# Kernel tuning notes

Measured on AMD Instinct MI355X. Metric: run time of the kernel, lower is better.

The kernel has to match this reference:

```python
import jax, jax.numpy as jnp
import numpy as np

E, MAX_M, K, N = 8, 2048, 2048, 8192

def setup_inputs() -> dict:
    key = jax.random.key(0)
    k1, k2, k3 = jax.random.split(key, 3)
    x_padded = jax.random.normal(k1, (E, MAX_M, K), dtype=jnp.float32)
    stacked_weights = jax.random.normal(k2, (E, N, K), dtype=jnp.float32) * 0.02
    m_sizes = jax.random.randint(k3, (E,), 0, MAX_M, dtype=jnp.int32)
    return {"x_padded": x_padded, "stacked_weights": stacked_weights, "m_sizes": m_sizes}

def reference(x_padded, stacked_weights, m_sizes):
    # valid-token mask per expert: [E, MAX_M]
    mask = (jnp.arange(MAX_M, dtype=jnp.int32)[None, :] < m_sizes[:, None])
    # zero padded rows (pad_expert_inputs fills with zeros)
    x = jnp.where(mask[:, :, None], x_padded, jnp.zeros((), x_padded.dtype))
    # grouped GEMM via batched matmul: [E, M, K] x [E, N, K]^T -> [E, M, N]
    out = jnp.einsum('emk,enk->emn', x, stacked_weights)
    # rows beyond m_sizes[i] are sliced away in the original; mask them to zero
    return jnp.where(mask[:, :, None], out, jnp.zeros((), out.dtype))
```

## Files before the change

kernel.cpp:

```cpp
#include <hip/hip_runtime.h>
#include <hip/hip_bf16.h>


#define NE   8
#define MAXM 2048
#define KD   2048
#define ND   8192

#define BM   256
#define BN   256
#define BK   64
#define NTS  (KD/BK)

typedef __attribute__((ext_vector_type(8))) short          short8;
typedef __attribute__((ext_vector_type(8))) unsigned short us8;
typedef __attribute__((ext_vector_type(4))) float          f32x4;
typedef __attribute__((ext_vector_type(4))) unsigned short us4;

__device__ __forceinline__ unsigned short f2bf(float f) {
    union { float f; unsigned u; } v; v.f = f;
    unsigned u = v.u;
    return (unsigned short)((u + 0x7FFFu + ((u >> 16) & 1u)) >> 16);
}

__device__ __forceinline__ void gload16(const void* g, void* l) {
    __builtin_amdgcn_global_load_lds(
        (const __attribute__((address_space(1))) void*)g,
        (__attribute__((address_space(3))) void*)l, 16, 0, 0);
}

__global__ __launch_bounds__(256) void cvt_kernel(const float* __restrict__ src,
                                                  unsigned short* __restrict__ dst,
                                                  int n8) {
    int i = blockIdx.x * blockDim.x + threadIdx.x;
    int stride = gridDim.x * blockDim.x;
    for (; i < n8; i += stride) {
        const f32x4* s = (const f32x4*)(src + (size_t)i * 8);
        f32x4 a = s[0], b = s[1];
        us8 v = (us8){f2bf(a[0]), f2bf(a[1]), f2bf(a[2]), f2bf(a[3]),
                      f2bf(b[0]), f2bf(b[1]), f2bf(b[2]), f2bf(b[3])};
        *(us8*)(dst + (size_t)i * 8) = v;
    }
}

__global__ __launch_bounds__(256) void cvt_x_kernel(const float* __restrict__ src,
                                                    unsigned short* __restrict__ dst,
                                                    const int* __restrict__ ms) {
    int bid = blockIdx.x;
    int e = bid >> 11, m = bid & 2047;
    if (m >= ms[e]) return;
    const float* s = src + ((size_t)e * MAXM + m) * KD;
    unsigned short* d = dst + ((size_t)e * MAXM + m) * KD;
    int t = threadIdx.x;
    const f32x4* s4 = (const f32x4*)(s + t * 8);
    f32x4 a = s4[0], b = s4[1];
    us8 v = (us8){f2bf(a[0]), f2bf(a[1]), f2bf(a[2]), f2bf(a[3]),
                  f2bf(b[0]), f2bf(b[1]), f2bf(b[2]), f2bf(b[3])};
    *(us8*)(d + t * 8) = v;
}

__global__ __launch_bounds__(512, 2) void ggemm_pers(
    const unsigned short* __restrict__ xb,
    const unsigned short* __restrict__ wb,
    const int*   __restrict__ ms,
    float*       __restrict__ out)
{
    int p    = blockIdx.x;
    int xcd  = p & 7;
    int q    = p >> 3;
    int rrot = q >> 2;
    int bc   = xcd * 4 + (q & 3);
    int col0 = bc * BN;
    int tid  = threadIdx.x;

    __shared__ int s_live[8];
    __shared__ int s_nlive;
    __shared__ unsigned short Ak[2][2][BM * 32];
    __shared__ unsigned short Bk[2][2][BN * 32];

    if (tid == 0) {
        int n = 0;
        #pragma unroll
        for (int e = 0; e < NE; ++e) {
            int br = (rrot + e) & 7;
            if (br * BM < ms[e]) { s_live[n] = (e << 3) | br; ++n; }
        }
        s_nlive = n;
    }

    #pragma unroll 1
    for (int e = 0; e < NE; ++e) {
        int br   = (rrot + e) & 7;
        int row0 = br * BM;
        if (row0 >= ms[e]) {
            float* outE = out + (size_t)e * MAXM * ND;
            f32x4 z = (f32x4){0.f, 0.f, 0.f, 0.f};
            #pragma unroll
            for (int j = 0; j < 32; ++j) {
                int i2 = tid + j * 512;
                int rr = i2 >> 6, cc = (i2 & 63) << 2;
                *(f32x4*)(outE + (size_t)(row0 + rr) * ND + col0 + cc) = z;
            }
        }
    }
    __syncthreads();
    int nlive = s_nlive;
    if (nlive == 0) return;

    int wid = tid >> 6, lane = tid & 63;
    int wr = wid >> 2, wc = wid & 3;
    int lr = lane & 15, kg = lane >> 4;
    int srow = lane >> 2;
    int ss   = (lane & 3) ^ ((lane >> 3) & 3);

    auto stageA = [&](int b, int kh, const unsigned short* xP, int kt) {
        #pragma unroll
        for (int j = 0; j < 2; ++j) {
            int blk = wid * 2 + j;
            const unsigned short* src =
                xP + (size_t)(blk * 16 + srow) * KD + kt * BK + kh * 32 + ss * 8;
            gload16(src, (char*)&Ak[b][kh][0] + blk * 1024);
        }
    };
    auto stageB = [&](int b, int kh, const unsigned short* wP, int kt) {
        #pragma unroll
        for (int j = 0; j < 2; ++j) {
            int blk = wid * 2 + j;
            const unsigned short* src =
                wP + (size_t)(blk * 16 + srow) * KD + kt * BK + kh * 32 + ss * 8;
            gload16(src, (char*)&Bk[b][kh][0] + blk * 1024);
        }
    };
    auto ldA = [&](short8* a, int b, int kh) {
        #pragma unroll
        for (int mf = 0; mf < 8; ++mf) {
            int row  = wr * 128 + mf * 16 + lr;
            int slot = kg ^ ((row >> 1) & 3);
            a[mf] = *(const short8*)&Ak[b][kh][row * 32 + slot * 8];
        }
    };
    auto ldB = [&](short8* bf, int b, int kh, int nh) {
        #pragma unroll
        for (int i = 0; i < 2; ++i) {
            int row  = wc * 64 + (nh * 2 + i) * 16 + lr;
            int slot = kg ^ ((row >> 1) & 3);
            bf[i] = *(const short8*)&Bk[b][kh][row * 32 + slot * 8];
        }
    };

    f32x4 acc[8][4];
    #pragma unroll
    for (int mf = 0; mf < 8; ++mf)
        #pragma unroll
        for (int nf = 0; nf < 4; ++nf)
            acc[mf][nf] = (f32x4){0.f, 0.f, 0.f, 0.f};

    const unsigned short *xC, *wC, *xN, *wN;
    float *oC, *oN;
    int msC, r0C, msN, r0N;
    {
        int v = s_live[0]; int e = v >> 3, br = v & 7;
        r0C = br * BM; msC = ms[e];
        xC = xb + ((size_t)e * MAXM + r0C) * KD;
        wC = wb + ((size_t)e * ND + col0) * KD;
        oC = out + (size_t)e * MAXM * ND;
    }
    if (nlive > 1) {
        int v = s_live[1]; int e = v >> 3, br = v & 7;
        r0N = br * BM; msN = ms[e];
        xN = xb + ((size_t)e * MAXM + r0N) * KD;
        wN = wb + ((size_t)e * ND + col0) * KD;
        oN = out + (size_t)e * MAXM * ND;
    } else { xN = xC; wN = wC; oN = oC; msN = msC; r0N = r0C; }

    stageA(0, 0, xC, 0); stageB(0, 0, wC, 0);
    stageA(0, 1, xC, 0); stageB(0, 1, wC, 0);
    stageA(1, 0, xC, 1); stageB(1, 0, wC, 1);
    asm volatile("s_waitcnt vmcnt(8)" ::: "memory");
    __builtin_amdgcn_s_barrier();

    #pragma unroll 1
    for (int s = 0; s < nlive; ++s) {
        bool last  = (s + 1 >= nlive);
        bool alive = (r0C + wr * 128) < msC;

        auto tile = [&](int b, int kt) {
            bool g1 = (kt + 1 < NTS) || (!last);
            bool g2 = (kt + 2 < NTS) || (!last);
            const unsigned short* xS1 = (kt + 1 < NTS) ? xC : xN;
            const unsigned short* wS1 = (kt + 1 < NTS) ? wC : wN;
            int k1 = (kt + 1 < NTS) ? kt + 1 : 0;
            const unsigned short* xS2 = (kt + 2 < NTS) ? xC : xN;
            const unsigned short* wS2 = (kt + 2 < NTS) ? wC : wN;
            int k2 = (kt + 2 < NTS) ? kt + 2 : kt + 2 - NTS;

            short8 a[8], bf[2];
            if (alive) { ldA(a, b, 0); ldB(bf, b, 0, 0); }
            if (g1) stageA(b ^ 1, 1, xS1, k1);
            __builtin_amdgcn_s_barrier();
            __builtin_amdgcn_s_setprio(1);
            if (alive) {
                #pragma unroll
                for (int mf = 0; mf < 8; ++mf) {
                    acc[mf][0] = __builtin_amdgcn_mfma_f32_16x16x32_bf16(a[mf], bf[0], acc[mf][0], 0, 0, 0);
                    acc[mf][1] = __builtin_amdgcn_mfma_f32_16x16x32_bf16(a[mf], bf[1], acc[mf][1], 0, 0, 0);
                }
            }
            __builtin_amdgcn_s_setprio(0);
            __builtin_amdgcn_s_barrier();
            if (alive) ldB(bf, b, 0, 1);
            if (g1) stageB(b ^ 1, 1, wS1, k1);
            __builtin_amdgcn_s_barrier();
            __builtin_amdgcn_s_setprio(1);
            if (alive) {
                #pragma unroll
                for (int mf = 0; mf < 8; ++mf) {
                    acc[mf][2] = __builtin_amdgcn_mfma_f32_16x16x32_bf16(a[mf], bf[0], acc[mf][2], 0, 0, 0);
                    acc[mf][3] = __builtin_amdgcn_mfma_f32_16x16x32_bf16(a[mf], bf[1], acc[mf][3], 0, 0, 0);
                }
            }
            __builtin_amdgcn_s_setprio(0);
            if (g1) { asm volatile("s_waitcnt vmcnt(8)" ::: "memory"); }
            else    { asm volatile("s_waitcnt vmcnt(0)" ::: "memory"); }
            __builtin_amdgcn_s_barrier();
            if (alive) { ldA(a, b, 1); ldB(bf, b, 1, 0); }
            if (g2) stageA(b, 0, xS2, k2);
            __builtin_amdgcn_s_barrier();
            __builtin_amdgcn_s_setprio(1);
            if (alive) {
                #pragma unroll
                for (int mf = 0; mf < 8; ++mf) {
                    acc[mf][0] = __builtin_amdgcn_mfma_f32_16x16x32_bf16(a[mf], bf[0], acc[mf][0], 0, 0, 0);
                    acc[mf][1] = __builtin_amdgcn_mfma_f32_16x16x32_bf16(a[mf], bf[1], acc[mf][1], 0, 0, 0);
                }
            }
            __builtin_amdgcn_s_setprio(0);
            __builtin_amdgcn_s_barrier();
            if (alive) ldB(bf, b, 1, 1);
            if (g2) stageB(b, 0, wS2, k2);
            __builtin_amdgcn_s_barrier();
            __builtin_amdgcn_s_setprio(1);
            if (alive) {
                #pragma unroll
                for (int mf = 0; mf < 8; ++mf) {
                    acc[mf][2] = __builtin_amdgcn_mfma_f32_16x16x32_bf16(a[mf], bf[0], acc[mf][2], 0, 0, 0);
                    acc[mf][3] = __builtin_amdgcn_mfma_f32_16x16x32_bf16(a[mf], bf[1], acc[mf][3], 0, 0, 0);
                }
            }
            __builtin_amdgcn_s_setprio(0);
            if (g2)      { asm volatile("s_waitcnt vmcnt(8)" ::: "memory"); }
            else if (g1) { asm volatile("s_waitcnt vmcnt(4)" ::: "memory"); }
            else         { asm volatile("s_waitcnt vmcnt(0)" ::: "memory"); }
            __builtin_amdgcn_s_barrier();
        };

        #pragma unroll 1
        for (int kt = 0; kt < NTS; kt += 2) {
            tile(0, kt);
            tile(1, kt + 1);
        }

        #pragma unroll
        for (int mf = 0; mf < 8; ++mf) {
            int rbase = r0C + wr * 128 + mf * 16 + kg * 4;
            #pragma unroll
            for (int nf = 0; nf < 4; ++nf) {
                int gc = col0 + wc * 64 + nf * 16 + lr;
                #pragma unroll
                for (int j = 0; j < 4; ++j) {
                    int gr = rbase + j;
                    float v = (gr < msC) ? acc[mf][nf][j] : 0.f;
                    oC[(size_t)gr * ND + gc] = v;
                    acc[mf][nf][j] = 0.f;
                }
            }
        }

        xC = xN; wC = wN; oC = oN; msC = msN; r0C = r0N;
        if (s + 2 < nlive) {
            int v = s_live[s + 2]; int e = v >> 3, br = v & 7;
            r0N = br * BM; msN = ms[e];
            xN = xb + ((size_t)e * MAXM + r0N) * KD;
            wN = wb + ((size_t)e * ND + col0) * KD;
            oN = out + (size_t)e * MAXM * ND;
        }
    }
}

#define FBM 128
#define FBK 32
#define FTM (MAXM/FBM)
#define FTN (ND/FBM)
#define FNT (KD/FBK)
#define LSTR 40
__global__ __launch_bounds__(256, 2) void ggemm_fused(
    const float* __restrict__ x, const float* __restrict__ w,
    const int* __restrict__ ms, float* __restrict__ out)
{
    int nwg  = gridDim.x;
    int orig = blockIdx.x;
    int cpx  = nwg >> 3;
    int bid  = (orig & 7) * cpx + (orig >> 3);
    int e   = bid / (FTM * FTN);
    int rem = bid % (FTM * FTN);
    int br  = rem % FTM;
    int bc  = rem / FTM;
    int m_size = ms[e];
    int row0 = br * FBM, col0 = bc * FBM;
    float* outE = out + (size_t)e * MAXM * ND;
    int tid = threadIdx.x;

    if (row0 >= m_size) {
        f32x4 z = (f32x4){0.f, 0.f, 0.f, 0.f};
        #pragma unroll
        for (int j = 0; j < 16; ++j) {
            int i2 = tid + j * 256;
            int rr = i2 >> 5, cc = (i2 & 31) << 2;
            *(f32x4*)(outE + (size_t)(row0 + rr) * ND + col0 + cc) = z;
        }
        return;
    }

    const float* xE = x + ((size_t)e * MAXM + row0) * KD;
    const float* wE = w + ((size_t)e * ND   + col0) * KD;

    __shared__ unsigned short As[2][FBM][LSTR];
    __shared__ unsigned short Bs[2][FBM][LSTR];

    int sr  = tid >> 3;
    int sc4 = tid & 7;
    int wid = tid >> 6, lane = tid & 63;
    int wr = wid >> 1, wc = wid & 1;
    int lr = lane & 15, kg = lane >> 4;

    f32x4 acc[4][4];
    #pragma unroll
    for (int m = 0; m < 4; ++m)
        #pragma unroll
        for (int n = 0; n < 4; ++n)
            acc[m][n] = (f32x4){0.f, 0.f, 0.f, 0.f};

    {
        #pragma unroll
        for (int j = 0; j < 4; ++j) {
            int r0 = sr + j * 32;
            f32x4 av = *(const f32x4*)(xE + (size_t)r0 * KD + sc4 * 4);
            f32x4 bv = *(const f32x4*)(wE + (size_t)r0 * KD + sc4 * 4);
            us4 ah = (us4){f2bf(av[0]), f2bf(av[1]), f2bf(av[2]), f2bf(av[3])};
            us4 bh = (us4){f2bf(bv[0]), f2bf(bv[1]), f2bf(bv[2]), f2bf(bv[3])};
            *(us4*)&As[0][r0][sc4 * 4] = ah;
            *(us4*)&Bs[0][r0][sc4 * 4] = bh;
        }
    }
    __syncthreads();

    for (int t = 0; t < FNT; ++t) {
        int cur = t & 1;
        f32x4 av[4], bv[4];
        bool pre = (t + 1 < FNT);
        if (pre) {
            const float* xk = xE + (size_t)(t + 1) * FBK;
            const float* wk = wE + (size_t)(t + 1) * FBK;
            #pragma unroll
            for (int j = 0; j < 4; ++j) {
                int r0 = sr + j * 32;
                av[j] = *(const f32x4*)(xk + (size_t)r0 * KD + sc4 * 4);
                bv[j] = *(const f32x4*)(wk + (size_t)r0 * KD + sc4 * 4);
            }
        }
        short8 a[4], b[4];
        #pragma unroll
        for (int m = 0; m < 4; ++m)
            a[m] = *(const short8*)&As[cur][wr * 64 + m * 16 + lr][kg * 8];
        #pragma unroll
        for (int n = 0; n < 4; ++n)
            b[n] = *(const short8*)&Bs[cur][wc * 64 + n * 16 + lr][kg * 8];
        #pragma unroll
        for (int m = 0; m < 4; ++m)
            #pragma unroll
            for (int n = 0; n < 4; ++n)
                acc[m][n] = __builtin_amdgcn_mfma_f32_16x16x32_bf16(a[m], b[n], acc[m][n], 0, 0, 0);

        if (pre) {
            int nb = cur ^ 1;
            #pragma unroll
            for (int j = 0; j < 4; ++j) {
                int r0 = sr + j * 32;
                us4 ah = (us4){f2bf(av[j][0]), f2bf(av[j][1]), f2bf(av[j][2]), f2bf(av[j][3])};
                us4 bh = (us4){f2bf(bv[j][0]), f2bf(bv[j][1]), f2bf(bv[j][2]), f2bf(bv[j][3])};
                *(us4*)&As[nb][r0][sc4 * 4] = ah;
                *(us4*)&Bs[nb][r0][sc4 * 4] = bh;
            }
        }
        __syncthreads();
    }

    #pragma unroll
    for (int m = 0; m < 4; ++m) {
        int rbase = row0 + wr * 64 + m * 16 + kg * 4;
        #pragma unroll
        for (int n = 0; n < 4; ++n) {
            int gc = col0 + wc * 64 + n * 16 + lr;
            #pragma unroll
            for (int j = 0; j < 4; ++j) {
                int gr = rbase + j;
                float v = (gr < m_size) ? acc[m][n][j] : 0.f;
                outE[(size_t)gr * ND + gc] = v;
            }
        }
    }
}

extern "C" void kernel_launch(void* const* d_in, const int* in_sizes, int n_in,
                              void* d_out, int out_size, void* d_ws, size_t ws_size,
                              hipStream_t stream) {
    const float* x  = (const float*)d_in[0];
    const float* w  = (const float*)d_in[1];
    const int*   ms = (const int*)d_in[2];
    float* out = (float*)d_out;

    const size_t xElems = (size_t)NE * MAXM * KD;
    const size_t wElems = (size_t)NE * ND   * KD;
    const size_t need   = (xElems + wElems) * 2;

    if (ws_size >= need) {
        unsigned short* xb = (unsigned short*)d_ws;
        unsigned short* wb = xb + xElems;
        cvt_x_kernel<<<NE * MAXM, 256, 0, stream>>>(x, xb, ms);
        cvt_kernel<<<2048, 256, 0, stream>>>(w, wb, (int)(wElems / 8));
        ggemm_pers<<<256, 512, 0, stream>>>(xb, wb, ms, out);
    } else {
        ggemm_fused<<<dim3(NE * (MAXM/FBM) * (ND/FBM)), dim3(256), 0, stream>>>(x, w, ms, out);
    }
}
```

Baseline: 583.9 us.

## Balance live tiles across persistent blocks and merge MFMA phases per k-half

Live and dead output tiles are now counted per expert and handed to the 32 persistent blocks per XCD round-robin, with columns chosen dynamically. Before, each block had a fixed column and a rotating row slot, which could leave blocks with uneven live-tile counts. The inner k-tile loop is also restructured: each k-half loads all four B fragments and runs 32 MFMAs in one phase, and the A and B stages are issued together. This halves the barriers per k-tile at the cost of more live registers and a coarser overlap of loads with compute.

```diff
diff --git a/kernel.cpp b/kernel.cpp
--- a/kernel.cpp
+++ b/kernel.cpp
@@ -65,46 +65,44 @@
     const int*   __restrict__ ms,
     float*       __restrict__ out)
 {
-    int p    = blockIdx.x;
-    int xcd  = p & 7;
-    int q    = p >> 3;
-    int rrot = q >> 2;
-    int bc   = xcd * 4 + (q & 3);
-    int col0 = bc * BN;
-    int tid  = threadIdx.x;
-
-    __shared__ int s_live[8];
-    __shared__ int s_nlive;
+    int p   = blockIdx.x;
+    int xcd = p & 7;
+    int jj  = p >> 3;
+    int tid = threadIdx.x;
+
+    __shared__ int s_live[8], s_dead[8], s_cnt[2];
     __shared__ unsigned short Ak[2][2][BM * 32];
     __shared__ unsigned short Bk[2][2][BN * 32];
 
     if (tid == 0) {
-        int n = 0;
+        int nl = 0, nd = 0, cumL = 0, cumD = 0, il = jj, id = jj;
         #pragma unroll
         for (int e = 0; e < NE; ++e) {
-            int br = (rrot + e) & 7;
-            if (br * BM < ms[e]) { s_live[n] = (e << 3) | br; ++n; }
-        }
-        s_nlive = n;
-    }
-
+            int L = (ms[e] + 255) >> 8;
+            int cntL = L << 2, cntD = (8 - L) << 2;
+            while (il < cumL + cntL) { int o = il - cumL; s_live[nl++] = (e << 5) | ((o >> 2) << 2) | (o & 3); il += 32; }
+            while (id < cumD + cntD) { int o = id - cumD; s_dead[nd++] = (e << 5) | ((L + (o >> 2)) << 2) | (o & 3); id += 32; }
+            cumL += cntL; cumD += cntD;
+        }
+        s_cnt[0] = nl; s_cnt[1] = nd;
+    }
+    __syncthreads();
+
+    int ndead = s_cnt[1];
     #pragma unroll 1
-    for (int e = 0; e < NE; ++e) {
-        int br   = (rrot + e) & 7;
-        int row0 = br * BM;
-        if (row0 >= ms[e]) {
-            float* outE = out + (size_t)e * MAXM * ND;
-            f32x4 z = (f32x4){0.f, 0.f, 0.f, 0.f};
-            #pragma unroll
-            for (int j = 0; j < 32; ++j) {
-                int i2 = tid + j * 512;
-                int rr = i2 >> 6, cc = (i2 & 63) << 2;
-                *(f32x4*)(outE + (size_t)(row0 + rr) * ND + col0 + cc) = z;
-            }
-        }
-    }
-    __syncthreads();
-    int nlive = s_nlive;
+    for (int d = 0; d < ndead; ++d) {
+        int v = s_dead[d]; int e = v >> 5, br = (v >> 2) & 7, bcl = v & 3;
+        float* outE = out + (size_t)e * MAXM * ND;
+        int row0 = br * BM, col0 = (xcd * 4 + bcl) * BN;
+        f32x4 z = (f32x4){0.f, 0.f, 0.f, 0.f};
+        #pragma unroll
+        for (int q = 0; q < 32; ++q) {
+            int i2 = tid + q * 512;
+            int rr = i2 >> 6, cc = (i2 & 63) << 2;
+            *(f32x4*)(outE + (size_t)(row0 + rr) * ND + col0 + cc) = z;
+        }
+    }
+    int nlive = s_cnt[0];
     if (nlive == 0) return;
 
     int wid = tid >> 6, lane = tid & 63;
@@ -115,8 +113,8 @@
 
     auto stageA = [&](int b, int kh, const unsigned short* xP, int kt) {
         #pragma unroll
-        for (int j = 0; j < 2; ++j) {
-            int blk = wid * 2 + j;
+        for (int q = 0; q < 2; ++q) {
+            int blk = wid * 2 + q;
             const unsigned short* src =
                 xP + (size_t)(blk * 16 + srow) * KD + kt * BK + kh * 32 + ss * 8;
             gload16(src, (char*)&Ak[b][kh][0] + blk * 1024);
@@ -124,8 +122,8 @@
     };
     auto stageB = [&](int b, int kh, const unsigned short* wP, int kt) {
         #pragma unroll
-        for (int j = 0; j < 2; ++j) {
-            int blk = wid * 2 + j;
+        for (int q = 0; q < 2; ++q) {
+            int blk = wid * 2 + q;
             const unsigned short* src =
                 wP + (size_t)(blk * 16 + srow) * KD + kt * BK + kh * 32 + ss * 8;
             gload16(src, (char*)&Bk[b][kh][0] + blk * 1024);
@@ -139,10 +137,10 @@
             a[mf] = *(const short8*)&Ak[b][kh][row * 32 + slot * 8];
         }
     };
-    auto ldB = [&](short8* bf, int b, int kh, int nh) {
-        #pragma unroll
-        for (int i = 0; i < 2; ++i) {
-            int row  = wc * 64 + (nh * 2 + i) * 16 + lr;
+    auto ldB4 = [&](short8* bf, int b, int kh) {
+        #pragma unroll
+        for (int i = 0; i < 4; ++i) {
+            int row  = wc * 64 + i * 16 + lr;
             int slot = kg ^ ((row >> 1) & 3);
             bf[i] = *(const short8*)&Bk[b][kh][row * 32 + slot * 8];
         }
@@ -157,21 +155,21 @@
 
     const unsigned short *xC, *wC, *xN, *wN;
     float *oC, *oN;
-    int msC, r0C, msN, r0N;
+    int msC, r0C, c0C, msN, r0N, c0N;
     {
-        int v = s_live[0]; int e = v >> 3, br = v & 7;
-        r0C = br * BM; msC = ms[e];
+        int v = s_live[0]; int e = v >> 5, br = (v >> 2) & 7, bcl = v & 3;
+        r0C = br * BM; c0C = (xcd * 4 + bcl) * BN; msC = ms[e];
         xC = xb + ((size_t)e * MAXM + r0C) * KD;
-        wC = wb + ((size_t)e * ND + col0) * KD;
+        wC = wb + ((size_t)e * ND + c0C) * KD;
         oC = out + (size_t)e * MAXM * ND;
     }
     if (nlive > 1) {
-        int v = s_live[1]; int e = v >> 3, br = v & 7;
-        r0N = br * BM; msN = ms[e];
+        int v = s_live[1]; int e = v >> 5, br = (v >> 2) & 7, bcl = v & 3;
+        r0N = br * BM; c0N = (xcd * 4 + bcl) * BN; msN = ms[e];
         xN = xb + ((size_t)e * MAXM + r0N) * KD;
-        wN = wb + ((size_t)e * ND + col0) * KD;
+        wN = wb + ((size_t)e * ND + c0N) * KD;
         oN = out + (size_t)e * MAXM * ND;
-    } else { xN = xC; wN = wC; oN = oC; msN = msC; r0N = r0C; }
+    } else { xN = xC; wN = wC; oN = oC; msN = msC; r0N = r0C; c0N = c0C; }
 
     stageA(0, 0, xC, 0); stageB(0, 0, wC, 0);
     stageA(0, 1, xC, 0); stageB(0, 1, wC, 0);
@@ -194,63 +192,36 @@
             const unsigned short* wS2 = (kt + 2 < NTS) ? wC : wN;
             int k2 = (kt + 2 < NTS) ? kt + 2 : kt + 2 - NTS;
 
-            short8 a[8], bf[2];
-            if (alive) { ldA(a, b, 0); ldB(bf, b, 0, 0); }
-            if (g1) stageA(b ^ 1, 1, xS1, k1);
+            short8 a[8], bf[4];
+            if (alive) { ldA(a, b, 0); ldB4(bf, b, 0); }
+            if (g1) { stageA(b ^ 1, 1, xS1, k1); stageB(b ^ 1, 1, wS1, k1); }
             __builtin_amdgcn_s_barrier();
             __builtin_amdgcn_s_setprio(1);
             if (alive) {
                 #pragma unroll
-                for (int mf = 0; mf < 8; ++mf) {
-                    acc[mf][0] = __builtin_amdgcn_mfma_f32_16x16x32_bf16(a[mf], bf[0], acc[mf][0], 0, 0, 0);
-                    acc[mf][1] = __builtin_amdgcn_mfma_f32_16x16x32_bf16(a[mf], bf[1], acc[mf][1], 0, 0, 0);
-                }
+                for (int mf = 0; mf < 8; ++mf)
+                    #pragma unroll
+                    for (int nf = 0; nf < 4; ++nf)
+                        acc[mf][nf] = __builtin_amdgcn_mfma_f32_16x16x32_bf16(a[mf], bf[nf], acc[mf][nf], 0, 0, 0);
             }
             __builtin_amdgcn_s_setprio(0);
+            if (g1) { asm volatile("s_waitcnt vmcnt(8)" ::: "memory"); }
+            else    { asm volatile("s_waitcnt vmcnt(0)" ::: "memory"); }
             __builtin_amdgcn_s_barrier();
-            if (alive) ldB(bf, b, 0, 1);
-            if (g1) stageB(b ^ 1, 1, wS1, k1);
+            if (alive) { ldA(a, b, 1); ldB4(bf, b, 1); }
+            if (g2) { stageA(b, 0, xS2, k2); stageB(b, 0, wS2, k2); }
             __builtin_amdgcn_s_barrier();
             __builtin_amdgcn_s_setprio(1);
             if (alive) {
                 #pragma unroll
-                for (int mf = 0; mf < 8; ++mf) {
-                    acc[mf][2] = __builtin_amdgcn_mfma_f32_16x16x32_bf16(a[mf], bf[0], acc[mf][2], 0, 0, 0);
-                    acc[mf][3] = __builtin_amdgcn_mfma_f32_16x16x32_bf16(a[mf], bf[1], acc[mf][3], 0, 0, 0);
-                }
+                for (int mf = 0; mf < 8; ++mf)
+                    #pragma unroll
+                    for (int nf = 0; nf < 4; ++nf)
+                        acc[mf][nf] = __builtin_amdgcn_mfma_f32_16x16x32_bf16(a[mf], bf[nf], acc[mf][nf], 0, 0, 0);
             }
             __builtin_amdgcn_s_setprio(0);
-            if (g1) { asm volatile("s_waitcnt vmcnt(8)" ::: "memory"); }
+            if (g2) { asm volatile("s_waitcnt vmcnt(8)" ::: "memory"); }
             else    { asm volatile("s_waitcnt vmcnt(0)" ::: "memory"); }
-            __builtin_amdgcn_s_barrier();
-            if (alive) { ldA(a, b, 1); ldB(bf, b, 1, 0); }
-            if (g2) stageA(b, 0, xS2, k2);
-            __builtin_amdgcn_s_barrier();
-            __builtin_amdgcn_s_setprio(1);
-            if (alive) {
-                #pragma unroll
-                for (int mf = 0; mf < 8; ++mf) {
-                    acc[mf][0] = __builtin_amdgcn_mfma_f32_16x16x32_bf16(a[mf], bf[0], acc[mf][0], 0, 0, 0);
-                    acc[mf][1] = __builtin_amdgcn_mfma_f32_16x16x32_bf16(a[mf], bf[1], acc[mf][1], 0, 0, 0);
-                }
-            }
-            __builtin_amdgcn_s_setprio(0);
-            __builtin_amdgcn_s_barrier();
-            if (alive) ldB(bf, b, 1, 1);
-            if (g2) stageB(b, 0, wS2, k2);
-            __builtin_amdgcn_s_barrier();
-            __builtin_amdgcn_s_setprio(1);
-            if (alive) {
-                #pragma unroll
-                for (int mf = 0; mf < 8; ++mf) {
-                    acc[mf][2] = __builtin_amdgcn_mfma_f32_16x16x32_bf16(a[mf], bf[0], acc[mf][2], 0, 0, 0);
-                    acc[mf][3] = __builtin_amdgcn_mfma_f32_16x16x32_bf16(a[mf], bf[1], acc[mf][3], 0, 0, 0);
-                }
-            }
-            __builtin_amdgcn_s_setprio(0);
-            if (g2)      { asm volatile("s_waitcnt vmcnt(8)" ::: "memory"); }
-            else if (g1) { asm volatile("s_waitcnt vmcnt(4)" ::: "memory"); }
-            else         { asm volatile("s_waitcnt vmcnt(0)" ::: "memory"); }
             __builtin_amdgcn_s_barrier();
         };
 
@@ -265,23 +236,23 @@
             int rbase = r0C + wr * 128 + mf * 16 + kg * 4;
             #pragma unroll
             for (int nf = 0; nf < 4; ++nf) {
-                int gc = col0 + wc * 64 + nf * 16 + lr;
+                int gc = c0C + wc * 64 + nf * 16 + lr;
                 #pragma unroll
-                for (int j = 0; j < 4; ++j) {
-                    int gr = rbase + j;
-                    float v = (gr < msC) ? acc[mf][nf][j] : 0.f;
+                for (int q = 0; q < 4; ++q) {
+                    int gr = rbase + q;
+                    float v = (gr < msC) ? acc[mf][nf][q] : 0.f;
                     oC[(size_t)gr * ND + gc] = v;
-                    acc[mf][nf][j] = 0.f;
+                    acc[mf][nf][q] = 0.f;
                 }
             }
         }
 
-        xC = xN; wC = wN; oC = oN; msC = msN; r0C = r0N;
+        xC = xN; wC = wN; oC = oN; msC = msN; r0C = r0N; c0C = c0N;
         if (s + 2 < nlive) {
-            int v = s_live[s + 2]; int e = v >> 3, br = v & 7;
-            r0N = br * BM; msN = ms[e];
+            int v = s_live[s + 2]; int e = v >> 5, br = (v >> 2) & 7, bcl = v & 3;
+            r0N = br * BM; c0N = (xcd * 4 + bcl) * BN; msN = ms[e];
             xN = xb + ((size_t)e * MAXM + r0N) * KD;
-            wN = wb + ((size_t)e * ND + col0) * KD;
+            wN = wb + ((size_t)e * ND + c0N) * KD;
             oN = out + (size_t)e * MAXM * ND;
         }
     }
@@ -313,8 +284,8 @@
     if (row0 >= m_size) {
         f32x4 z = (f32x4){0.f, 0.f, 0.f, 0.f};
         #pragma unroll
-        for (int j = 0; j < 16; ++j) {
-            int i2 = tid + j * 256;
+        for (int q = 0; q < 16; ++q) {
+            int i2 = tid + q * 256;
             int rr = i2 >> 5, cc = (i2 & 31) << 2;
             *(f32x4*)(outE + (size_t)(row0 + rr) * ND + col0 + cc) = z;
         }
@@ -342,8 +313,8 @@
 
     {
         #pragma unroll
-        for (int j = 0; j < 4; ++j) {
-            int r0 = sr + j * 32;
+        for (int q = 0; q < 4; ++q) {
+            int r0 = sr + q * 32;
             f32x4 av = *(const f32x4*)(xE + (size_t)r0 * KD + sc4 * 4);
             f32x4 bv = *(const f32x4*)(wE + (size_t)r0 * KD + sc4 * 4);
             us4 ah = (us4){f2bf(av[0]), f2bf(av[1]), f2bf(av[2]), f2bf(av[3])};
@@ -362,10 +333,10 @@
             const float* xk = xE + (size_t)(t + 1) * FBK;
             const float* wk = wE + (size_t)(t + 1) * FBK;
             #pragma unroll
-            for (int j = 0; j < 4; ++j) {
-                int r0 = sr + j * 32;
-                av[j] = *(const f32x4*)(xk + (size_t)r0 * KD + sc4 * 4);
-                bv[j] = *(const f32x4*)(wk + (size_t)r0 * KD + sc4 * 4);
+            for (int q = 0; q < 4; ++q) {
+                int r0 = sr + q * 32;
+                av[q] = *(const f32x4*)(xk + (size_t)r0 * KD + sc4 * 4);
+                bv[q] = *(const f32x4*)(wk + (size_t)r0 * KD + sc4 * 4);
             }
         }
         short8 a[4], b[4];
@@ -384,10 +355,10 @@
         if (pre) {
             int nb = cur ^ 1;
             #pragma unroll
-            for (int j = 0; j < 4; ++j) {
-                int r0 = sr + j * 32;
-                us4 ah = (us4){f2bf(av[j][0]), f2bf(av[j][1]), f2bf(av[j][2]), f2bf(av[j][3])};
-                us4 bh = (us4){f2bf(bv[j][0]), f2bf(bv[j][1]), f2bf(bv[j][2]), f2bf(bv[j][3])};
+            for (int q = 0; q < 4; ++q) {
+                int r0 = sr + q * 32;
+                us4 ah = (us4){f2bf(av[q][0]), f2bf(av[q][1]), f2bf(av[q][2]), f2bf(av[q][3])};
+                us4 bh = (us4){f2bf(bv[q][0]), f2bf(bv[q][1]), f2bf(bv[q][2]), f2bf(bv[q][3])};
                 *(us4*)&As[nb][r0][sc4 * 4] = ah;
                 *(us4*)&Bs[nb][r0][sc4 * 4] = bh;
             }
@@ -402,9 +373,9 @@
         for (int n = 0; n < 4; ++n) {
             int gc = col0 + wc * 64 + n * 16 + lr;
             #pragma unroll
-            for (int j = 0; j < 4; ++j) {
-                int gr = rbase + j;
-                float v = (gr < m_size) ? acc[m][n][j] : 0.f;
+            for (int q = 0; q < 4; ++q) {
+                int gr = rbase + q;
+                float v = (gr < m_size) ? acc[m][n][q] : 0.f;
                 outE[(size_t)gr * ND + gc] = v;
             }
         }
```

Measured after the change: 581.2 us. Within noise of the previous version (-0.4%).
